# Performance work log

Measured on AMD Instinct MI355X. Metric: run time of the kernel, lower is better.

## Reference

```python
import jax, jax.numpy as jnp
import numpy as np

EMBED_DIM = 256
HIDDEN_DIM = 128
NUM_VARS = 1024


def _linear_params(key, fan_in, fan_out):
    kw, kb = jax.random.split(key)
    lim = 1.0 / np.sqrt(fan_in)
    W = jax.random.uniform(kw, (fan_in, fan_out), minval=-lim, maxval=lim, dtype=jnp.float32)
    b = jax.random.uniform(kb, (fan_out,), minval=-lim, maxval=lim, dtype=jnp.float32)
    return W, b


def setup_inputs() -> dict:
    key = jax.random.key(0)
    ks = jax.random.split(key, 7)
    next_state_embedding = jax.random.normal(ks[0], (EMBED_DIM,), dtype=jnp.float32)
    prev_variable_embeddings = jax.random.normal(ks[1], (NUM_VARS, EMBED_DIM), dtype=jnp.float32)
    Wq, bq = _linear_params(ks[2], EMBED_DIM, HIDDEN_DIM)
    Wk, bk = _linear_params(ks[3], EMBED_DIM, HIDDEN_DIM)
    Wc, bc = _linear_params(ks[4], EMBED_DIM, HIDDEN_DIM)
    W1, b1 = _linear_params(ks[5], 2 * HIDDEN_DIM, HIDDEN_DIM)
    W2, b2 = _linear_params(ks[6], HIDDEN_DIM, 1)
    return {
        "next_state_embedding": next_state_embedding,
        "prev_variable_embeddings": prev_variable_embeddings,
        "Wq": Wq, "bq": bq,
        "Wk": Wk, "bk": bk,
        "Wc": Wc, "bc": bc,
        "W1": W1, "b1": b1,
        "W2": W2, "b2": b2,
    }


def reference(next_state_embedding, prev_variable_embeddings,
              Wq, bq, Wk, bk, Wc, bc, W1, b1, W2, b2):
    n = prev_variable_embeddings.shape[0]
    h = Wq.shape[1]
    # context_net: Linear + ReLU on next-state embedding -> [h]
    context = jax.nn.relu(next_state_embedding @ Wc + bc)
    # queries/keys over prev vars, each shifted by context -> [n, h]
    queries = prev_variable_embeddings @ Wq + bq + context
    keys = prev_variable_embeddings @ Wk + bk + context
    # pair_scorer layer 1 on concat(q_i, k_j) decomposes:
    # hidden[i,j] = relu(q_i @ W1[:h] + k_j @ W1[h:] + b1)
    q_proj = queries @ W1[:h]            # [n, h]
    k_proj = keys @ W1[h:]               # [n, h]
    hidden = jax.nn.relu(q_proj[:, None, :] + k_proj[None, :, :] + b1)  # [n, n, h]
    scores = jnp.squeeze(hidden @ W2, axis=-1) + b2[0]  # [n, n]
    # extract i < j pairs in row-major order (matches the nested loop)
    iu, ju = jnp.triu_indices(n, k=1)
    return scores[iu, ju]  # [n*(n-1)/2]
```

## Files before the change

kernel.cpp:

```cpp
#include <hip/hip_runtime.h>

#define N 1024
#define E 256
#define H 128

typedef _Float16 hv2 __attribute__((ext_vector_type(2)));
typedef _Float16 half_t;

__device__ __forceinline__ float dot2_acc(hv2 a, hv2 b, float c) {
#if __has_builtin(__builtin_amdgcn_fdot2)
    return __builtin_amdgcn_fdot2(a, b, c, false);
#else
    return c + (float)a.x * (float)b.x + (float)a.y * (float)b.y;
#endif
}

__device__ __forceinline__ hv2 relu_add2(hv2 a, hv2 b) {
    hv2 s = a + b;
    hv2 z = (hv2)(_Float16)0.f;
    return __builtin_elementwise_max(s, z);
}

__global__ __launch_bounds__(256) void proj_kernel(
    const float* __restrict__ x, const float* __restrict__ P,
    const float* __restrict__ Wq, const float* __restrict__ bq,
    const float* __restrict__ Wk, const float* __restrict__ bk,
    const float* __restrict__ Wc, const float* __restrict__ bc,
    const float* __restrict__ W1, const float* __restrict__ b1,
    half_t* __restrict__ qh, half_t* __restrict__ kh) {
    __shared__ __align__(16) float xs[E];
    __shared__ __align__(16) float p_s[2 * E];
    __shared__ float pc[2 * H];
    __shared__ float aq[H], ak[H];
    __shared__ float sv[2][2 * H];

    int b = blockIdx.x, t = threadIdx.x;
    int i0 = b * 2;
    if (t < 64) ((float4*)xs)[t] = ((const float4*)x)[t];
    else if (t < 192) ((float4*)p_s)[t - 64] = ((const float4*)(P + i0 * E))[t - 64];
    __syncthreads();

    int h = t & (H - 1);
    int c = t >> 7;
    {
        float p = 0.f;
#pragma unroll 8
        for (int e = c * H; e < c * H + H; ++e) p += xs[e] * Wc[e * H + h];
        pc[c * H + h] = p;
    }
    __syncthreads();
    if (t < H) {
        float ctxv = fmaxf(pc[t] + pc[H + t] + bc[t], 0.f);
        aq[t] = bq[t] + ctxv;
        ak[t] = bk[t] + ctxv;
    }
    __syncthreads();

    {
        const float* W = c ? Wk : Wq;
        float a0 = c ? ak[h] : aq[h];
        float a1 = a0;
        for (int e = 0; e < E; e += 8) {
            float m0 = W[(e + 0) * H + h];
            float m1 = W[(e + 1) * H + h];
            float m2 = W[(e + 2) * H + h];
            float m3 = W[(e + 3) * H + h];
            float m4 = W[(e + 4) * H + h];
            float m5 = W[(e + 5) * H + h];
            float m6 = W[(e + 6) * H + h];
            float m7 = W[(e + 7) * H + h];
            float4 p0a = *(const float4*)&p_s[0 * E + e];
            float4 p0b = *(const float4*)&p_s[0 * E + e + 4];
            float4 p1a = *(const float4*)&p_s[1 * E + e];
            float4 p1b = *(const float4*)&p_s[1 * E + e + 4];
            a0 += p0a.x * m0 + p0a.y * m1 + p0a.z * m2 + p0a.w * m3
                + p0b.x * m4 + p0b.y * m5 + p0b.z * m6 + p0b.w * m7;
            a1 += p1a.x * m0 + p1a.y * m1 + p1a.z * m2 + p1a.w * m3
                + p1b.x * m4 + p1b.y * m5 + p1b.z * m6 + p1b.w * m7;
        }
        sv[0][c * H + h] = a0;
        sv[1][c * H + h] = a1;
    }
    __syncthreads();

    {
        const float* W1c = W1 + c * H * H;
        const float* S0 = &sv[0][c * H];
        const float* S1 = &sv[1][c * H];
        float a0 = c ? 0.f : b1[h];
        float a1 = a0;
        for (int r = 0; r < H; r += 8) {
            float w0 = W1c[(r + 0) * H + h];
            float w1 = W1c[(r + 1) * H + h];
            float w2 = W1c[(r + 2) * H + h];
            float w3 = W1c[(r + 3) * H + h];
            float w4 = W1c[(r + 4) * H + h];
            float w5 = W1c[(r + 5) * H + h];
            float w6 = W1c[(r + 6) * H + h];
            float w7 = W1c[(r + 7) * H + h];
            a0 += S0[r + 0] * w0 + S0[r + 1] * w1 + S0[r + 2] * w2 + S0[r + 3] * w3
                + S0[r + 4] * w4 + S0[r + 5] * w5 + S0[r + 6] * w6 + S0[r + 7] * w7;
            a1 += S1[r + 0] * w0 + S1[r + 1] * w1 + S1[r + 2] * w2 + S1[r + 3] * w3
                + S1[r + 4] * w4 + S1[r + 5] * w5 + S1[r + 6] * w6 + S1[r + 7] * w7;
        }
        half_t* O = c ? kh : qh;
        O[(i0 + 0) * H + h] = (half_t)a0;
        O[(i0 + 1) * H + h] = (half_t)a1;
    }
}

#define QSTR 136
__global__ __launch_bounds__(256) void pair_kernel(
    const half_t* __restrict__ qh, const half_t* __restrict__ kh,
    const float* __restrict__ W2, const float* __restrict__ b2,
    float* __restrict__ out) {
    int tid = blockIdx.x;
    int bi = (int)((65.0f - sqrtf(4225.0f - 8.0f * (float)tid)) * 0.5f);
    while (bi > 0 && tid < 32 * bi - bi * (bi - 1) / 2) --bi;
    while (tid >= 32 * (bi + 1) - (bi + 1) * bi / 2) ++bi;
    int bj = bi + (tid - (32 * bi - bi * (bi - 1) / 2));

    __shared__ __align__(16) half_t qs[32][QSTR];
    __shared__ __align__(16) half_t ks[32][QSTR];
    __shared__ __align__(16) half_t w2s[H];

    int t = threadIdx.x;
    if (t < H) w2s[t] = (half_t)W2[t];

    const float4* qh4 = (const float4*)(qh + bi * 32 * H);
    const float4* kh4 = (const float4*)(kh + bj * 32 * H);
#pragma unroll
    for (int v = 0; v < 2; ++v) {
        int idx = v * 256 + t;
        int r = idx >> 4, c = idx & 15;
        float4 q = qh4[idx];
        float4 k = kh4[idx];
        *(float4*)&qs[r][c * 8] = q;
        *(float4*)&ks[r][c * 8] = k;
    }
    __syncthreads();

    int jj  = t & 31;
    int ti0 = t >> 5;
    float b2v = b2[0];
    float acc[4];
#pragma unroll
    for (int u = 0; u < 4; ++u) acc[u] = b2v;

    for (int h8 = 0; h8 < 16; ++h8) {
        float4 wf = *(const float4*)&w2s[h8 * 8];
        float4 kv = *(const float4*)&ks[jj][h8 * 8];
        const hv2* wp = (const hv2*)&wf;
        const hv2* kp2 = (const hv2*)&kv;
#pragma unroll
        for (int u = 0; u < 4; ++u) {
            float4 qf = *(const float4*)&qs[ti0 + u * 8][h8 * 8];
            const hv2* qp2 = (const hv2*)&qf;
#pragma unroll
            for (int s = 0; s < 4; ++s) {
                hv2 sa = relu_add2(qp2[s], kp2[s]);
                acc[u] = dot2_acc(sa, wp[s], acc[u]);
            }
        }
    }

#pragma unroll
    for (int u = 0; u < 4; ++u) {
        int i = bi * 32 + ti0 + u * 8;
        int j = bj * 32 + jj;
        if (j > i) {
            int base = i * (2 * N - i - 1) / 2;
            out[base + (j - i - 1)] = acc[u];
        }
    }
}

extern "C" void kernel_launch(void* const* d_in, const int* in_sizes, int n_in,
                              void* d_out, int out_size, void* d_ws, size_t ws_size,
                              hipStream_t stream) {
    const float* x  = (const float*)d_in[0];
    const float* P  = (const float*)d_in[1];
    const float* Wq = (const float*)d_in[2];
    const float* bq = (const float*)d_in[3];
    const float* Wk = (const float*)d_in[4];
    const float* bk = (const float*)d_in[5];
    const float* Wc = (const float*)d_in[6];
    const float* bc = (const float*)d_in[7];
    const float* W1 = (const float*)d_in[8];
    const float* b1 = (const float*)d_in[9];
    const float* W2 = (const float*)d_in[10];
    const float* b2 = (const float*)d_in[11];
    float* out = (float*)d_out;

    half_t* qh = (half_t*)d_ws;
    half_t* kh = qh + N * H;

    proj_kernel<<<N / 2, 256, 0, stream>>>(x, P, Wq, bq, Wk, bk, Wc, bc, W1, b1,
                                           qh, kh);
    pair_kernel<<<528, 256, 0, stream>>>(qh, kh, W2, b2, out);
}
```

Before: 99.27 us.

## Fuse projection and pair kernels into one cooperative kernel with grid barrier

Merges the projection kernel and the pair-scoring kernel into a single cooperative launch of 528 blocks. A hand-written grid-wide barrier built from striped atomic counters separates the two phases, and shared memory is reused between them. This removes one kernel launch and the gap between launches. In exchange it adds a memset of the barrier area, the cost of the barrier spin, and a cooperative-launch requirement that all blocks be resident at once.

```diff
diff --git a/kernel.cpp b/kernel.cpp
--- a/kernel.cpp
+++ b/kernel.cpp
@@ -3,6 +3,8 @@
 #define N 1024
 #define E 256
 #define H 128
+#define NBLK 528
+#define QSTR 136
 
 typedef _Float16 hv2 __attribute__((ext_vector_type(2)));
 typedef _Float16 half_t;
@@ -21,156 +23,185 @@
     return __builtin_elementwise_max(s, z);
 }
 
-__global__ __launch_bounds__(256) void proj_kernel(
+__device__ __forceinline__ void full_barrier(int* bar) {
+    __syncthreads();
+    if (threadIdx.x == 0) {
+        __threadfence();
+        atomicAdd(&bar[(blockIdx.x & 31) * 32], 1);
+        if (blockIdx.x == 0) {
+            int total;
+            do {
+                total = 0;
+#pragma unroll
+                for (int i = 0; i < 32; ++i)
+                    total += __hip_atomic_load(&bar[i * 32], __ATOMIC_RELAXED,
+                                               __HIP_MEMORY_SCOPE_AGENT);
+            } while (total < NBLK);
+            __threadfence();
+            __hip_atomic_store(&bar[32 * 32], 1, __ATOMIC_RELEASE,
+                               __HIP_MEMORY_SCOPE_AGENT);
+        }
+        while (__hip_atomic_load(&bar[32 * 32], __ATOMIC_RELAXED,
+                                 __HIP_MEMORY_SCOPE_AGENT) == 0) {}
+        __threadfence();
+    }
+    __syncthreads();
+}
+
+__global__ __launch_bounds__(256, 3) void fused_kernel(
     const float* __restrict__ x, const float* __restrict__ P,
     const float* __restrict__ Wq, const float* __restrict__ bq,
     const float* __restrict__ Wk, const float* __restrict__ bk,
     const float* __restrict__ Wc, const float* __restrict__ bc,
     const float* __restrict__ W1, const float* __restrict__ b1,
-    half_t* __restrict__ qh, half_t* __restrict__ kh) {
-    __shared__ __align__(16) float xs[E];
-    __shared__ __align__(16) float p_s[2 * E];
-    __shared__ float pc[2 * H];
-    __shared__ float aq[H], ak[H];
-    __shared__ float sv[2][2 * H];
-
-    int b = blockIdx.x, t = threadIdx.x;
-    int i0 = b * 2;
-    if (t < 64) ((float4*)xs)[t] = ((const float4*)x)[t];
-    else if (t < 192) ((float4*)p_s)[t - 64] = ((const float4*)(P + i0 * E))[t - 64];
-    __syncthreads();
-
-    int h = t & (H - 1);
-    int c = t >> 7;
-    {
-        float p = 0.f;
-#pragma unroll 8
-        for (int e = c * H; e < c * H + H; ++e) p += xs[e] * Wc[e * H + h];
-        pc[c * H + h] = p;
-    }
-    __syncthreads();
-    if (t < H) {
-        float ctxv = fmaxf(pc[t] + pc[H + t] + bc[t], 0.f);
-        aq[t] = bq[t] + ctxv;
-        ak[t] = bk[t] + ctxv;
-    }
-    __syncthreads();
-
-    {
-        const float* W = c ? Wk : Wq;
-        float a0 = c ? ak[h] : aq[h];
-        float a1 = a0;
-        for (int e = 0; e < E; e += 8) {
-            float m0 = W[(e + 0) * H + h];
-            float m1 = W[(e + 1) * H + h];
-            float m2 = W[(e + 2) * H + h];
-            float m3 = W[(e + 3) * H + h];
-            float m4 = W[(e + 4) * H + h];
-            float m5 = W[(e + 5) * H + h];
-            float m6 = W[(e + 6) * H + h];
-            float m7 = W[(e + 7) * H + h];
-            float4 p0a = *(const float4*)&p_s[0 * E + e];
-            float4 p0b = *(const float4*)&p_s[0 * E + e + 4];
-            float4 p1a = *(const float4*)&p_s[1 * E + e];
-            float4 p1b = *(const float4*)&p_s[1 * E + e + 4];
-            a0 += p0a.x * m0 + p0a.y * m1 + p0a.z * m2 + p0a.w * m3
-                + p0b.x * m4 + p0b.y * m5 + p0b.z * m6 + p0b.w * m7;
-            a1 += p1a.x * m0 + p1a.y * m1 + p1a.z * m2 + p1a.w * m3
-                + p1b.x * m4 + p1b.y * m5 + p1b.z * m6 + p1b.w * m7;
-        }
-        sv[0][c * H + h] = a0;
-        sv[1][c * H + h] = a1;
-    }
-    __syncthreads();
-
-    {
-        const float* W1c = W1 + c * H * H;
-        const float* S0 = &sv[0][c * H];
-        const float* S1 = &sv[1][c * H];
-        float a0 = c ? 0.f : b1[h];
-        float a1 = a0;
-        for (int r = 0; r < H; r += 8) {
-            float w0 = W1c[(r + 0) * H + h];
-            float w1 = W1c[(r + 1) * H + h];
-            float w2 = W1c[(r + 2) * H + h];
-            float w3 = W1c[(r + 3) * H + h];
-            float w4 = W1c[(r + 4) * H + h];
-            float w5 = W1c[(r + 5) * H + h];
-            float w6 = W1c[(r + 6) * H + h];
-            float w7 = W1c[(r + 7) * H + h];
-            a0 += S0[r + 0] * w0 + S0[r + 1] * w1 + S0[r + 2] * w2 + S0[r + 3] * w3
-                + S0[r + 4] * w4 + S0[r + 5] * w5 + S0[r + 6] * w6 + S0[r + 7] * w7;
-            a1 += S1[r + 0] * w0 + S1[r + 1] * w1 + S1[r + 2] * w2 + S1[r + 3] * w3
-                + S1[r + 4] * w4 + S1[r + 5] * w5 + S1[r + 6] * w6 + S1[r + 7] * w7;
-        }
-        half_t* O = c ? kh : qh;
-        O[(i0 + 0) * H + h] = (half_t)a0;
-        O[(i0 + 1) * H + h] = (half_t)a1;
-    }
-}
-
-#define QSTR 136
-__global__ __launch_bounds__(256) void pair_kernel(
-    const half_t* __restrict__ qh, const half_t* __restrict__ kh,
     const float* __restrict__ W2, const float* __restrict__ b2,
+    int* bar,
+    half_t* __restrict__ qh, half_t* __restrict__ kh,
     float* __restrict__ out) {
-    int tid = blockIdx.x;
-    int bi = (int)((65.0f - sqrtf(4225.0f - 8.0f * (float)tid)) * 0.5f);
-    while (bi > 0 && tid < 32 * bi - bi * (bi - 1) / 2) --bi;
-    while (tid >= 32 * (bi + 1) - (bi + 1) * bi / 2) ++bi;
-    int bj = bi + (tid - (32 * bi - bi * (bi - 1) / 2));
-
     __shared__ __align__(16) half_t qs[32][QSTR];
     __shared__ __align__(16) half_t ks[32][QSTR];
     __shared__ __align__(16) half_t w2s[H];
-
-    int t = threadIdx.x;
-    if (t < H) w2s[t] = (half_t)W2[t];
-
-    const float4* qh4 = (const float4*)(qh + bi * 32 * H);
-    const float4* kh4 = (const float4*)(kh + bj * 32 * H);
-#pragma unroll
-    for (int v = 0; v < 2; ++v) {
-        int idx = v * 256 + t;
-        int r = idx >> 4, c = idx & 15;
-        float4 q = qh4[idx];
-        float4 k = kh4[idx];
-        *(float4*)&qs[r][c * 8] = q;
-        *(float4*)&ks[r][c * 8] = k;
+    float* fs  = (float*)&qs[0][0];
+    float* xs  = fs;
+    float* p_s = fs + 256;
+    float* pc  = fs + 768;
+    float* aq  = fs + 1024;
+    float* ak  = fs + 1152;
+    float* sv  = fs + 1280;
+
+    int b = blockIdx.x, t = threadIdx.x;
+    int h = t & (H - 1);
+    int c = t >> 7;
+
+    if (b < N / 2) {
+        int i0 = b * 2;
+        if (t < 64) ((float4*)xs)[t] = ((const float4*)x)[t];
+        else if (t < 192) ((float4*)p_s)[t - 64] = ((const float4*)(P + i0 * E))[t - 64];
+        __syncthreads();
+
+        {
+            float p = 0.f;
+#pragma unroll 8
+            for (int e = c * H; e < c * H + H; ++e) p += xs[e] * Wc[e * H + h];
+            pc[c * H + h] = p;
+        }
+        __syncthreads();
+        if (t < H) {
+            float ctxv = fmaxf(pc[t] + pc[H + t] + bc[t], 0.f);
+            aq[t] = bq[t] + ctxv;
+            ak[t] = bk[t] + ctxv;
+        }
+        __syncthreads();
+
+        {
+            const float* W = c ? Wk : Wq;
+            float a0 = c ? ak[h] : aq[h];
+            float a1 = a0;
+            for (int e = 0; e < E; e += 8) {
+                float m0 = W[(e + 0) * H + h];
+                float m1 = W[(e + 1) * H + h];
+                float m2 = W[(e + 2) * H + h];
+                float m3 = W[(e + 3) * H + h];
+                float m4 = W[(e + 4) * H + h];
+                float m5 = W[(e + 5) * H + h];
+                float m6 = W[(e + 6) * H + h];
+                float m7 = W[(e + 7) * H + h];
+                float4 p0a = *(const float4*)&p_s[0 * E + e];
+                float4 p0b = *(const float4*)&p_s[0 * E + e + 4];
+                float4 p1a = *(const float4*)&p_s[1 * E + e];
+                float4 p1b = *(const float4*)&p_s[1 * E + e + 4];
+                a0 += p0a.x * m0 + p0a.y * m1 + p0a.z * m2 + p0a.w * m3
+                    + p0b.x * m4 + p0b.y * m5 + p0b.z * m6 + p0b.w * m7;
+                a1 += p1a.x * m0 + p1a.y * m1 + p1a.z * m2 + p1a.w * m3
+                    + p1b.x * m4 + p1b.y * m5 + p1b.z * m6 + p1b.w * m7;
+            }
+            sv[0 * 2 * H + c * H + h] = a0;
+            sv[1 * 2 * H + c * H + h] = a1;
+        }
+        __syncthreads();
+
+        {
+            const float* W1c = W1 + c * H * H;
+            const float* S0 = sv + 0 * 2 * H + c * H;
+            const float* S1 = sv + 1 * 2 * H + c * H;
+            float a0 = c ? 0.f : b1[h];
+            float a1 = a0;
+            for (int r = 0; r < H; r += 8) {
+                float w0 = W1c[(r + 0) * H + h];
+                float w1 = W1c[(r + 1) * H + h];
+                float w2 = W1c[(r + 2) * H + h];
+                float w3 = W1c[(r + 3) * H + h];
+                float w4 = W1c[(r + 4) * H + h];
+                float w5 = W1c[(r + 5) * H + h];
+                float w6 = W1c[(r + 6) * H + h];
+                float w7 = W1c[(r + 7) * H + h];
+                a0 += S0[r + 0] * w0 + S0[r + 1] * w1 + S0[r + 2] * w2 + S0[r + 3] * w3
+                    + S0[r + 4] * w4 + S0[r + 5] * w5 + S0[r + 6] * w6 + S0[r + 7] * w7;
+                a1 += S1[r + 0] * w0 + S1[r + 1] * w1 + S1[r + 2] * w2 + S1[r + 3] * w3
+                    + S1[r + 4] * w4 + S1[r + 5] * w5 + S1[r + 6] * w6 + S1[r + 7] * w7;
+            }
+            half_t* O = c ? kh : qh;
+            O[(i0 + 0) * H + h] = (half_t)a0;
+            O[(i0 + 1) * H + h] = (half_t)a1;
+        }
     }
-    __syncthreads();
-
-    int jj  = t & 31;
-    int ti0 = t >> 5;
-    float b2v = b2[0];
-    float acc[4];
-#pragma unroll
-    for (int u = 0; u < 4; ++u) acc[u] = b2v;
-
-    for (int h8 = 0; h8 < 16; ++h8) {
-        float4 wf = *(const float4*)&w2s[h8 * 8];
-        float4 kv = *(const float4*)&ks[jj][h8 * 8];
-        const hv2* wp = (const hv2*)&wf;
-        const hv2* kp2 = (const hv2*)&kv;
+
+    full_barrier(bar);
+
+    {
+        int tid = b;
+        int bi = (int)((65.0f - sqrtf(4225.0f - 8.0f * (float)tid)) * 0.5f);
+        while (bi > 0 && tid < 32 * bi - bi * (bi - 1) / 2) --bi;
+        while (tid >= 32 * (bi + 1) - (bi + 1) * bi / 2) ++bi;
+        int bj = bi + (tid - (32 * bi - bi * (bi - 1) / 2));
+
+        if (t < H) w2s[t] = (half_t)W2[t];
+        float b2v = b2[0];
+
+        const float4* qh4 = (const float4*)(qh + bi * 32 * H);
+        const float4* kh4 = (const float4*)(kh + bj * 32 * H);
+#pragma unroll
+        for (int v = 0; v < 2; ++v) {
+            int idx = v * 256 + t;
+            int r = idx >> 4, cc = idx & 15;
+            float4 q = qh4[idx];
+            float4 k = kh4[idx];
+            *(float4*)&qs[r][cc * 8] = q;
+            *(float4*)&ks[r][cc * 8] = k;
+        }
+        __syncthreads();
+
+        int jj  = t & 31;
+        int ti0 = t >> 5;
+        float acc[4];
+#pragma unroll
+        for (int u = 0; u < 4; ++u) acc[u] = b2v;
+
+        for (int h8 = 0; h8 < 16; ++h8) {
+            float4 wf = *(const float4*)&w2s[h8 * 8];
+            float4 kv = *(const float4*)&ks[jj][h8 * 8];
+            const hv2* wp = (const hv2*)&wf;
+            const hv2* kp2 = (const hv2*)&kv;
+#pragma unroll
+            for (int u = 0; u < 4; ++u) {
+                float4 qf = *(const float4*)&qs[ti0 + u * 8][h8 * 8];
+                const hv2* qp2 = (const hv2*)&qf;
+#pragma unroll
+                for (int s = 0; s < 4; ++s) {
+                    hv2 sa = relu_add2(qp2[s], kp2[s]);
+                    acc[u] = dot2_acc(sa, wp[s], acc[u]);
+                }
+            }
+        }
+
 #pragma unroll
         for (int u = 0; u < 4; ++u) {
-            float4 qf = *(const float4*)&qs[ti0 + u * 8][h8 * 8];
-            const hv2* qp2 = (const hv2*)&qf;
-#pragma unroll
-            for (int s = 0; s < 4; ++s) {
-                hv2 sa = relu_add2(qp2[s], kp2[s]);
-                acc[u] = dot2_acc(sa, wp[s], acc[u]);
-            }
-        }
-    }
-
-#pragma unroll
-    for (int u = 0; u < 4; ++u) {
-        int i = bi * 32 + ti0 + u * 8;
-        int j = bj * 32 + jj;
-        if (j > i) {
-            int base = i * (2 * N - i - 1) / 2;
-            out[base + (j - i - 1)] = acc[u];
+            int i = bi * 32 + ti0 + u * 8;
+            int j = bj * 32 + jj;
+            if (j > i) {
+                int base = i * (2 * N - i - 1) / 2;
+                out[base + (j - i - 1)] = acc[u];
+            }
         }
     }
 }
@@ -192,10 +223,16 @@
     const float* b2 = (const float*)d_in[11];
     float* out = (float*)d_out;
 
-    half_t* qh = (half_t*)d_ws;
+    int* bar   = (int*)d_ws;
+    half_t* qh = (half_t*)((char*)d_ws + 8192);
     half_t* kh = qh + N * H;
 
-    proj_kernel<<<N / 2, 256, 0, stream>>>(x, P, Wq, bq, Wk, bk, Wc, bc, W1, b1,
-                                           qh, kh);
-    pair_kernel<<<528, 256, 0, stream>>>(qh, kh, W2, b2, out);
-}
+    hipMemsetAsync(d_ws, 0, 8192, stream);
+
+    void* args[] = {
+        (void*)&x,  (void*)&P,  (void*)&Wq, (void*)&bq, (void*)&Wk, (void*)&bk,
+        (void*)&Wc, (void*)&bc, (void*)&W1, (void*)&b1, (void*)&W2, (void*)&b2,
+        (void*)&bar, (void*)&qh, (void*)&kh, (void*)&out};
+    hipLaunchCooperativeKernel((const void*)fused_kernel, dim3(NBLK), dim3(256),
+                               args, 0, stream);
+}
```

Measured after the change: 151.0 us. 1.52x slower.

## Restructure projection kernel: 4 rows per block, split q/k side and K-dim across halves

Applied to the files above, without the earlier changes.

Each projection block now handles one side (query or key) for four rows instead of both sides for two rows. The two thread halves split the reduction dimension and combine partial sums through shared memory. Each weight element loaded from global memory is reused across four rows instead of two, and each thread runs half as many loop iterations, which cuts per-row weight traffic. The cost is extra shared-memory reductions and barriers, and the context projection is still recomputed in every block.

```diff
diff --git a/kernel.cpp b/kernel.cpp
--- a/kernel.cpp
+++ b/kernel.cpp
@@ -29,38 +29,42 @@
     const float* __restrict__ W1, const float* __restrict__ b1,
     half_t* __restrict__ qh, half_t* __restrict__ kh) {
     __shared__ __align__(16) float xs[E];
-    __shared__ __align__(16) float p_s[2 * E];
-    __shared__ float pc[2 * H];
-    __shared__ float aq[H], ak[H];
-    __shared__ float sv[2][2 * H];
+    __shared__ __align__(16) float p_s[4 * E];
+    __shared__ float pc[2][H];
+    __shared__ float av[H];
+    __shared__ float sp[2][4][H];
+    __shared__ float sv[4][H];
+    __shared__ float qpp[2][4][H];
 
     int b = blockIdx.x, t = threadIdx.x;
-    int i0 = b * 2;
+    int side = b & 1;
+    int i0 = (b >> 1) * 4;
+    int h = t & (H - 1);
+    int g = t >> 7;
+
     if (t < 64) ((float4*)xs)[t] = ((const float4*)x)[t];
-    else if (t < 192) ((float4*)p_s)[t - 64] = ((const float4*)(P + i0 * E))[t - 64];
-    __syncthreads();
-
-    int h = t & (H - 1);
-    int c = t >> 7;
-    {
+    ((float4*)p_s)[t] = ((const float4*)(P + i0 * E))[t];
+    __syncthreads();
+
+    {
+        const float* Wce = Wc + g * H * H;
+        const float* xg = xs + g * H;
         float p = 0.f;
 #pragma unroll 8
-        for (int e = c * H; e < c * H + H; ++e) p += xs[e] * Wc[e * H + h];
-        pc[c * H + h] = p;
+        for (int e = 0; e < H; ++e) p += xg[e] * Wce[e * H + h];
+        pc[g][h] = p;
     }
     __syncthreads();
     if (t < H) {
-        float ctxv = fmaxf(pc[t] + pc[H + t] + bc[t], 0.f);
-        aq[t] = bq[t] + ctxv;
-        ak[t] = bk[t] + ctxv;
-    }
-    __syncthreads();
-
-    {
-        const float* W = c ? Wk : Wq;
-        float a0 = c ? ak[h] : aq[h];
-        float a1 = a0;
-        for (int e = 0; e < E; e += 8) {
+        float ctxv = fmaxf(pc[0][t] + pc[1][t] + bc[t], 0.f);
+        av[t] = (side ? bk[t] : bq[t]) + ctxv;
+    }
+    __syncthreads();
+
+    {
+        const float* W = (side ? Wk : Wq) + g * H * H;
+        float a0 = 0.f, a1 = 0.f, a2 = 0.f, a3 = 0.f;
+        for (int e = 0; e < H; e += 8) {
             float m0 = W[(e + 0) * H + h];
             float m1 = W[(e + 1) * H + h];
             float m2 = W[(e + 2) * H + h];
@@ -69,27 +73,33 @@
             float m5 = W[(e + 5) * H + h];
             float m6 = W[(e + 6) * H + h];
             float m7 = W[(e + 7) * H + h];
-            float4 p0a = *(const float4*)&p_s[0 * E + e];
-            float4 p0b = *(const float4*)&p_s[0 * E + e + 4];
-            float4 p1a = *(const float4*)&p_s[1 * E + e];
-            float4 p1b = *(const float4*)&p_s[1 * E + e + 4];
-            a0 += p0a.x * m0 + p0a.y * m1 + p0a.z * m2 + p0a.w * m3
-                + p0b.x * m4 + p0b.y * m5 + p0b.z * m6 + p0b.w * m7;
-            a1 += p1a.x * m0 + p1a.y * m1 + p1a.z * m2 + p1a.w * m3
-                + p1b.x * m4 + p1b.y * m5 + p1b.z * m6 + p1b.w * m7;
-        }
-        sv[0][c * H + h] = a0;
-        sv[1][c * H + h] = a1;
-    }
-    __syncthreads();
-
-    {
-        const float* W1c = W1 + c * H * H;
-        const float* S0 = &sv[0][c * H];
-        const float* S1 = &sv[1][c * H];
-        float a0 = c ? 0.f : b1[h];
-        float a1 = a0;
-        for (int r = 0; r < H; r += 8) {
+#pragma unroll
+            for (int r = 0; r < 4; ++r) {
+                float4 pa = *(const float4*)&p_s[r * E + g * H + e];
+                float4 pb = *(const float4*)&p_s[r * E + g * H + e + 4];
+                float v = pa.x * m0 + pa.y * m1 + pa.z * m2 + pa.w * m3
+                        + pb.x * m4 + pb.y * m5 + pb.z * m6 + pb.w * m7;
+                if (r == 0) a0 += v; else if (r == 1) a1 += v;
+                else if (r == 2) a2 += v; else a3 += v;
+            }
+        }
+        sp[g][0][h] = a0;
+        sp[g][1][h] = a1;
+        sp[g][2][h] = a2;
+        sp[g][3][h] = a3;
+    }
+    __syncthreads();
+    {
+        int r0 = g * 2, r1 = r0 + 1;
+        sv[r0][h] = sp[0][r0][h] + sp[1][r0][h] + av[h];
+        sv[r1][h] = sp[0][r1][h] + sp[1][r1][h] + av[h];
+    }
+    __syncthreads();
+
+    {
+        const float* W1c = W1 + (side * H + g * 64) * H;
+        float a0 = 0.f, a1 = 0.f, a2 = 0.f, a3 = 0.f;
+        for (int r = 0; r < 64; r += 8) {
             float w0 = W1c[(r + 0) * H + h];
             float w1 = W1c[(r + 1) * H + h];
             float w2 = W1c[(r + 2) * H + h];
@@ -98,14 +108,29 @@
             float w5 = W1c[(r + 5) * H + h];
             float w6 = W1c[(r + 6) * H + h];
             float w7 = W1c[(r + 7) * H + h];
-            a0 += S0[r + 0] * w0 + S0[r + 1] * w1 + S0[r + 2] * w2 + S0[r + 3] * w3
-                + S0[r + 4] * w4 + S0[r + 5] * w5 + S0[r + 6] * w6 + S0[r + 7] * w7;
-            a1 += S1[r + 0] * w0 + S1[r + 1] * w1 + S1[r + 2] * w2 + S1[r + 3] * w3
-                + S1[r + 4] * w4 + S1[r + 5] * w5 + S1[r + 6] * w6 + S1[r + 7] * w7;
-        }
-        half_t* O = c ? kh : qh;
-        O[(i0 + 0) * H + h] = (half_t)a0;
-        O[(i0 + 1) * H + h] = (half_t)a1;
+#pragma unroll
+            for (int rr = 0; rr < 4; ++rr) {
+                const float* S = &sv[rr][g * 64 + r];
+                float v = S[0] * w0 + S[1] * w1 + S[2] * w2 + S[3] * w3
+                        + S[4] * w4 + S[5] * w5 + S[6] * w6 + S[7] * w7;
+                if (rr == 0) a0 += v; else if (rr == 1) a1 += v;
+                else if (rr == 2) a2 += v; else a3 += v;
+            }
+        }
+        qpp[g][0][h] = a0;
+        qpp[g][1][h] = a1;
+        qpp[g][2][h] = a2;
+        qpp[g][3][h] = a3;
+    }
+    __syncthreads();
+    {
+        float bb = side ? 0.f : b1[h];
+        int r0 = g * 2, r1 = r0 + 1;
+        float v0 = qpp[0][r0][h] + qpp[1][r0][h] + bb;
+        float v1 = qpp[0][r1][h] + qpp[1][r1][h] + bb;
+        half_t* O = side ? kh : qh;
+        O[(i0 + r0) * H + h] = (half_t)v0;
+        O[(i0 + r1) * H + h] = (half_t)v1;
     }
 }
 
@@ -195,7 +220,7 @@
     half_t* qh = (half_t*)d_ws;
     half_t* kh = qh + N * H;
 
-    proj_kernel<<<N / 2, 256, 0, stream>>>(x, P, Wq, bq, Wk, bk, Wc, bc, W1, b1,
-                                           qh, kh);
+    proj_kernel<<<512, 256, 0, stream>>>(x, P, Wq, bq, Wk, bk, Wc, bc, W1, b1,
+                                         qh, kh);
     pair_kernel<<<528, 256, 0, stream>>>(qh, kh, W2, b2, out);
 }
```

After: 96.35 us. 2.9% less time.
